# Kernel tuning notes

Measured on AMD Instinct MI355X. Metric: run time of the kernel, lower is better.

Reference implementation:

```python
import jax, jax.numpy as jnp
import numpy as np

HID = 4544; NH = 71; NKV = 1; HD = 64  # Falcon-7B MQA geometry (head_dim hardcoded 64 in _split_heads)
B = 1; U = 32; C = 4; S = 2048          # batch, users, kv chunks, chunk length


def rotate_half(x):
    d = x.shape[-1] // 2
    return jnp.concatenate((-x[..., d:], x[..., :d]), axis=-1)


def setup_inputs() -> dict:
    key = jax.random.key(0)
    ks = jax.random.split(key, 7)
    hidden_states = jax.random.normal(ks[0], (B, U, HID), jnp.float32)
    cos = jax.random.uniform(ks[1], (1, U, 1, HD), jnp.float32, -1.0, 1.0)
    sin = jax.random.uniform(ks[2], (1, U, 1, HD), jnp.float32, -1.0, 1.0)
    k_cache = jax.random.normal(ks[3], (C, B, U, S, HD), jnp.float32)
    v_cache = jax.random.normal(ks[4], (C, B, U, S, HD), jnp.float32)
    attn_masks = jnp.zeros((C, B, U, S), jnp.float32)
    w_qkv = jax.random.normal(ks[5], ((NKV * (NH // NKV + 2)) * HD, HID), jnp.float32) * 0.02
    w_dense = jax.random.normal(ks[6], (HID, HID), jnp.float32) * 0.02
    return {"hidden_states": hidden_states, "cos": cos, "sin": sin,
            "k_cache": k_cache, "v_cache": v_cache, "attn_masks": attn_masks,
            "w_qkv": w_qkv, "w_dense": w_dense}


def reference(hidden_states, cos, sin, k_cache, v_cache, attn_masks, w_qkv, w_dense):
    b, u, _ = hidden_states.shape
    # fused QKV projection (Linear without bias: x @ W.T)
    fused = hidden_states @ w_qkv.T                      # [b,u,(NH+2*NKV)*HD]
    qkv = fused.reshape(b, u, NKV, NH // NKV + 2, HD)    # _split_heads view
    q = qkv[:, :, :, :-2].reshape(b, u, NH, HD)          # query heads
    k_cur = qkv[:, :, :, -2].reshape(b, u, NKV, HD)      # shared MQA key head
    v_cur = qkv[:, :, :, -1].reshape(b, u, NKV, HD)      # shared MQA value head
    # rotary embedding (apply_rotary_pos_emb)
    q = q * cos + rotate_half(q) * sin
    k_cur = k_cur * cos + rotate_half(k_cur) * sin
    inv = 1.0 / jnp.sqrt(jnp.float32(HD))
    # flash-decode over cached chunks: scores [c,b,u,n,s]
    scores = jnp.einsum('bund,cbusd->cbuns', q, k_cache) * inv
    scores = scores + attn_masks[:, :, :, None, :]
    m_c = jnp.max(scores, axis=-1, keepdims=True)        # [c,b,u,n,1] local max
    p = jnp.exp(scores - m_c)
    l_c = jnp.sum(p, axis=-1, keepdims=True)             # local row sums
    # current token = length-1 chunk (its local max is itself, local sum is 1)
    s_cur = jnp.einsum('bund,bued->bune', q, k_cur) * inv  # [b,u,n,1]
    g = jnp.maximum(jnp.max(m_c, axis=0), s_cur)           # global max [b,u,n,1]
    factor = jnp.exp(m_c - g[None])                        # per-chunk rescale
    out = jnp.einsum('cbuns,cbusd->bund', factor * p, v_cache)
    cur_w = jnp.exp(s_cur - g)                             # [b,u,n,1]
    out = out + cur_w * v_cur                              # v_cur broadcasts over heads
    scale = jnp.sum(factor * l_c, axis=0) + cur_w
    out = out / scale
    attn = out.reshape(b, u, NH * HD)
    return attn @ w_dense.T
```

## Files before the change

### kernel.cpp

```cpp
#include <hip/hip_runtime.h>
#include <hip/hip_bf16.h>

typedef __bf16 bf16_t;
typedef __bf16 bf16x8 __attribute__((ext_vector_type(8)));
typedef float  f32x4  __attribute__((ext_vector_type(4)));

#define MFMA16(A,B,C) __builtin_amdgcn_mfma_f32_16x16x32_bf16(A,B,C,0,0,0)

constexpr int HIDc = 4544;
constexpr int NHc  = 71;
constexpr int NHPc = 80;
constexpr int HDc  = 64;
constexpr int Uc   = 32;
constexpr int Sc   = 2048;
constexpr int RQ   = 4672;

constexpr size_t OFF_FUSED = 0;
constexpr size_t OFF_QHI   = 598016;
constexpr size_t OFF_QLO   = 925696;
constexpr size_t OFF_KCUR  = 1253376;
constexpr size_t OFF_VCUR  = 1261568;
constexpr size_t OFF_MP    = 1269760;
constexpr size_t OFF_LP    = 1415168;
constexpr size_t OFF_AHI   = 1560576;
constexpr size_t OFF_ALO   = 1851392;
constexpr size_t OFF_OP    = 2142208;

__device__ __forceinline__ bf16x8 ld8f(const float* base, long eidx) {
  const float* p = base + eidx;
  const f32x4 a = *(const f32x4*)p;
  const f32x4 b = *(const f32x4*)(p + 4);
  bf16x8 r;
  r[0]=(bf16_t)a[0]; r[1]=(bf16_t)a[1]; r[2]=(bf16_t)a[2]; r[3]=(bf16_t)a[3];
  r[4]=(bf16_t)b[0]; r[5]=(bf16_t)b[1]; r[6]=(bf16_t)b[2]; r[7]=(bf16_t)b[3];
  return r;
}

__device__ __forceinline__ void cp16(const float* g, float* l) {
  __builtin_amdgcn_global_load_lds((const __attribute__((address_space(1))) void*)g,
                                   (__attribute__((address_space(3))) void*)l, 16, 0, 0);
}
__device__ __forceinline__ void cp4(const float* g, float* l) {
  __builtin_amdgcn_global_load_lds((const __attribute__((address_space(1))) void*)g,
                                   (__attribute__((address_space(3))) void*)l, 4, 0, 0);
}

__global__ __launch_bounds__(256) void k_zeros(float* fused, float* out) {
  const int i = blockIdx.x*256 + threadIdx.x;
  if (i < Uc*RQ) fused[i] = 0.f;
  else           out[i - Uc*RQ] = 0.f;
}

__global__ __launch_bounds__(256) void k_qkv(
    const float* __restrict__ hidden, const float* __restrict__ wqkv,
    float* __restrict__ fused)
{
  const int h = blockIdx.x, y = blockIdx.y;
  const int t = threadIdx.x;
  const int wave = t >> 6, lane = t & 63;
  const int c = lane & 15, q4 = lane >> 4;
  const int mt = wave & 1, kh = wave >> 1;
  const int ks0 = y*18;
  const int ksn = min(18, 142 - ks0);
  const int h1  = ksn >> 1;
  const int kbeg = ks0 + (kh ? h1 : 0);
  const int kend = ks0 + (kh ? ksn : h1);
  __shared__ float sD[Uc*HDc];

  const long abase = (long)(mt*16 + c)*HIDc + q4*8;
  const long bbase = ((long)h*64 + c)*HIDc + q4*8;
  f32x4 acc[4] = {};
#pragma unroll 3
  for (int ks = kbeg; ks < kend; ++ks) {
    const bf16x8 af = ld8f(hidden, abase + ks*32);
#pragma unroll
    for (int nf = 0; nf < 4; ++nf) {
      const bf16x8 bv = ld8f(wqkv, bbase + (long)nf*16*HIDc + ks*32);
      acc[nf] = MFMA16(af, bv, acc[nf]);
    }
  }
  if (kh == 0) {
#pragma unroll
    for (int r = 0; r < 4; ++r)
#pragma unroll
      for (int nf = 0; nf < 4; ++nf)
        sD[(mt*16 + q4*4 + r)*64 + nf*16 + c] = acc[nf][r];
  }
  __syncthreads();
  if (kh == 1) {
#pragma unroll
    for (int r = 0; r < 4; ++r)
#pragma unroll
      for (int nf = 0; nf < 4; ++nf)
        sD[(mt*16 + q4*4 + r)*64 + nf*16 + c] += acc[nf][r];
  }
  __syncthreads();
  for (int i = t; i < Uc*HDc; i += 256)
    atomicAdd(&fused[(long)(i >> 6)*RQ + h*64 + (i & 63)], sD[i]);
}

__global__ __launch_bounds__(256) void k_rotary(
    const float* __restrict__ fused,
    const float* __restrict__ cosp, const float* __restrict__ sinp,
    bf16_t* __restrict__ qhi, bf16_t* __restrict__ qlo,
    float* __restrict__ kcur, float* __restrict__ vcur)
{
  const int h = blockIdx.x;
  const int t = threadIdx.x;
  __shared__ float sD[Uc*HDc];
  if (h < 73) {
    for (int i = t; i < Uc*HDc; i += 256)
      sD[i] = fused[(long)(i >> 6)*RQ + h*64 + (i & 63)];
    __syncthreads();
  }
  if (h >= NHc) {
    for (int i = t; i < Uc*HDc; i += 256) {
      const long idx = (((long)(i >> 6))*NHPc + h)*HDc + (i & 63);
      qhi[idx] = (bf16_t)0.f;  qlo[idx] = (bf16_t)0.f;
    }
  }
  if (h >= 73) return;
  for (int i = t; i < Uc*HDc; i += 256) {
    const int u = i >> 6, d = i & 63;
    const float x = sD[i];
    const float partner = sD[i ^ 32];
    const float cs = cosp[u*HDc + d];
    const float sn = sinp[u*HDc + d];
    const float rh = (d < 32) ? -partner : partner;
    const float val = x*cs + rh*sn;
    if (h < NHc) {
      const long idx = ((long)u*NHPc + h)*HDc + d;
      const bf16_t hi = (bf16_t)val;
      qhi[idx] = hi;
      qlo[idx] = (bf16_t)(val - (float)hi);
    } else if (h == NHc) {
      kcur[u*HDc + d] = val;
    } else {
      vcur[u*HDc + d] = x;
    }
  }
}

constexpr int ATTN_SLOT_F   = 4096;
constexpr int ATTN_STAGE_F  = 4*ATTN_SLOT_F;
constexpr int ATTN_SMEM_F   = ATTN_STAGE_F + 2048;
constexpr int ATTN_SMEM_BYTES = ATTN_SMEM_F * 4;

__global__ __launch_bounds__(512, 4) void k_attn(
    const float* __restrict__ kc, const float* __restrict__ vc,
    const float* __restrict__ masks,
    const bf16_t* __restrict__ qhi, const bf16_t* __restrict__ qlo,
    float* __restrict__ Mp, float* __restrict__ Lp, float* __restrict__ Op,
    const int NPB)
{
  extern __shared__ float smem[];
  const int u  = blockIdx.x;
  const int pb = blockIdx.y;
  const int tid = threadIdx.x;
  const int wave = __builtin_amdgcn_readfirstlane(tid >> 6);
  const int lane = tid & 63;
  const int c    = lane & 15;
  const int q4   = lane >> 4;
  const int pbpc = NPB >> 2;
  const int keys_pb = 2048 / pbpc;
  const int tcnt    = keys_pb >> 5;
  const int chunk = pb / pbpc;
  const int inner = pb - chunk*pbpc;
  const int s_base = inner*keys_pb;
  const long kvbase = ((long)(chunk*Uc + u))*Sc;

  float* const stage = smem;
  float* const smask = smem + ATTN_STAGE_F;

  const int srow = lane >> 4;
  const int scol = (lane & 15) << 2;

  if (wave >= 5) {
    if (wave == 7) {
      const int nmc = keys_pb >> 6;
      const float* gM = masks + kvbase + s_base;
      for (int i = 0; i < nmc; ++i)
        cp4(gM + i*64 + lane, smask + i*64);
      for (int t = 0; t < tcnt; ++t) {
        __builtin_amdgcn_s_barrier();
        if (t == 0) asm volatile("s_waitcnt vmcnt(0)" ::: "memory");
        __builtin_amdgcn_s_barrier();
      }
      return;
    }
    const float* gsrc = (wave == 5) ? kc : vc;
    const int vofs = (wave == 6) ? 2048 : 0;
    for (int pt = 0; pt < 3; ++pt) {
      const long tb = (kvbase + s_base + pt*32) * 64;
      float* dst = stage + pt*ATTN_SLOT_F + vofs;
#pragma unroll
      for (int i = 0; i < 8; ++i) {
        const int row = i*4 + srow;
        const int fz = ((row & 7) << 2) ^ (((row >> 3) & 1) << 4);
        cp16(gsrc + tb + row*64 + (scol ^ fz), dst + i*256);
      }
    }
    for (int t = 0; t < tcnt; ++t) {
      __builtin_amdgcn_s_barrier();
      if (t + 3 < tcnt) {
        const long tb = (kvbase + s_base + (long)(t+3)*32) * 64;
        float* dst = stage + ((t+3)&3)*ATTN_SLOT_F + vofs;
#pragma unroll
        for (int i = 0; i < 8; ++i) {
          const int row = i*4 + srow;
          const int fz = ((row & 7) << 2) ^ (((row >> 3) & 1) << 4);
          cp16(gsrc + tb + row*64 + (scol ^ fz), dst + i*256);
        }
      }
      const int rem = min(3, tcnt - 1 - t);
      if      (rem >= 3) asm volatile("s_waitcnt vmcnt(24)" ::: "memory");
      else if (rem == 2) asm volatile("s_waitcnt vmcnt(16)" ::: "memory");
      else if (rem == 1) asm volatile("s_waitcnt vmcnt(8)"  ::: "memory");
      else               asm volatile("s_waitcnt vmcnt(0)"  ::: "memory");
      __builtin_amdgcn_s_barrier();
    }
    return;
  }

  const int ht = wave;
  bf16x8 qh[2], ql[2];
  {
    const bf16_t* qb  = qhi + ((long)u*NHPc + ht*16 + c)*HDc + q4*8;
    const bf16_t* qb2 = qlo + ((long)u*NHPc + ht*16 + c)*HDc + q4*8;
#pragma unroll
    for (int ks = 0; ks < 2; ++ks) {
      qh[ks] = *(const bf16x8*)(qb  + ks*32);
      ql[ks] = *(const bf16x8*)(qb2 + ks*32);
    }
  }

  float m_i = -INFINITY, l_i = 0.f;
  f32x4 Oa[4] = {};

  const int krow0 = ((c >> 2) << 3) + (c & 3);

  for (int t = 0; t < tcnt; ++t) {
    __syncthreads();
    __syncthreads();
    float* const lK = stage + (t & 3)*ATTN_SLOT_F;
    float* const lV = lK + 2048;

    bf16x8 kf[2][2];
#pragma unroll
    for (int mt2 = 0; mt2 < 2; ++mt2) {
      const int row = krow0 + mt2*4;
      const int fz = ((row & 7) << 2) ^ (((row >> 3) & 1) << 4);
#pragma unroll
      for (int ks = 0; ks < 2; ++ks) {
        const int b0 = row*64 + ((ks*32 + q4*8) ^ fz);
        const int b1 = row*64 + ((ks*32 + q4*8 + 4) ^ fz);
        const f32x4 a = *(const f32x4*)(lK + b0);
        const f32x4 b = *(const f32x4*)(lK + b1);
        bf16x8 r;
        r[0]=(bf16_t)a[0]; r[1]=(bf16_t)a[1]; r[2]=(bf16_t)a[2]; r[3]=(bf16_t)a[3];
        r[4]=(bf16_t)b[0]; r[5]=(bf16_t)b[1]; r[6]=(bf16_t)b[2]; r[7]=(bf16_t)b[3];
        kf[mt2][ks] = r;
      }
    }

    bf16x8 vf[4];
#pragma unroll
    for (int dt = 0; dt < 4; ++dt) {
      union { bf16_t e[8]; bf16x8 v; } uv;
#pragma unroll
      for (int j = 0; j < 8; ++j) {
        const int row = q4*8 + j;
        const int fz = ((row & 7) << 2) ^ (((row >> 3) & 1) << 4);
        uv.e[j] = (bf16_t)lV[row*64 + ((dt*16 + c) ^ fz)];
      }
      vf[dt] = uv.v;
    }

    f32x4 S[2];
#pragma unroll
    for (int mt2 = 0; mt2 < 2; ++mt2) {
      f32x4 s = {};
      s = MFMA16(kf[mt2][0], qh[0], s);
      s = MFMA16(kf[mt2][1], qh[1], s);
      s = MFMA16(kf[mt2][0], ql[0], s);
      s = MFMA16(kf[mt2][1], ql[1], s);
      S[mt2] = s;
    }

#pragma unroll
    for (int mt2 = 0; mt2 < 2; ++mt2)
#pragma unroll
      for (int r = 0; r < 4; ++r)
        S[mt2][r] = S[mt2][r]*0.125f + smask[t*32 + q4*8 + mt2*4 + r];

    float tm = S[0][0];
#pragma unroll
    for (int mt2 = 0; mt2 < 2; ++mt2)
#pragma unroll
      for (int r = 0; r < 4; ++r) tm = fmaxf(tm, S[mt2][r]);
    tm = fmaxf(tm, __shfl_xor(tm, 16));
    tm = fmaxf(tm, __shfl_xor(tm, 32));
    const float mn = fmaxf(m_i, tm);
    const float alpha = __expf(m_i - mn);
    m_i = mn;
#pragma unroll
    for (int mt2 = 0; mt2 < 2; ++mt2)
#pragma unroll
      for (int r = 0; r < 4; ++r)
        S[mt2][r] = __expf(S[mt2][r] - m_i);
    float rs = 0.f;
#pragma unroll
    for (int mt2 = 0; mt2 < 2; ++mt2)
#pragma unroll
      for (int r = 0; r < 4; ++r) rs += S[mt2][r];
    rs += __shfl_xor(rs, 16);
    rs += __shfl_xor(rs, 32);
    l_i = l_i*alpha + rs;

#pragma unroll
    for (int r = 0; r < 4; ++r) {
      const float ar = __shfl(alpha, q4*4 + r);
#pragma unroll
      for (int dt = 0; dt < 4; ++dt) Oa[dt][r] *= ar;
    }
    bf16x8 ph, pl;
    {
      union { bf16_t e[8]; bf16x8 v; } uh, ul;
#pragma unroll
      for (int j = 0; j < 8; ++j) {
        const float val = (j < 4) ? S[0][j] : S[1][j & 3];
        const bf16_t hi = (bf16_t)val;
        uh.e[j] = hi;
        ul.e[j] = (bf16_t)(val - (float)hi);
      }
      ph = uh.v;  pl = ul.v;
    }
#pragma unroll
    for (int dt = 0; dt < 4; ++dt) {
      Oa[dt] = MFMA16(ph, vf[dt], Oa[dt]);
      Oa[dt] = MFMA16(pl, vf[dt], Oa[dt]);
    }
  }

  float* op = Op + ((long)u*NPB + pb)*NHc*HDc;
#pragma unroll
  for (int dt = 0; dt < 4; ++dt)
#pragma unroll
    for (int r = 0; r < 4; ++r) {
      const int h = ht*16 + q4*4 + r;
      if (h < NHc) op[h*HDc + dt*16 + c] = Oa[dt][r];
    }
  if (q4 == 0) {
    const int hh = ht*16 + c;
    if (hh < NHc) {
      Mp[((long)u*NPB + pb)*NHc + hh] = fmaxf(m_i, -1e30f);
      Lp[((long)u*NPB + pb)*NHc + hh] = l_i;
    }
  }
}

__global__ __launch_bounds__(64) void k_combine(
    const float* __restrict__ Mp, const float* __restrict__ Lp,
    const float* __restrict__ Op,
    const bf16_t* __restrict__ qhi, const bf16_t* __restrict__ qlo,
    const float* __restrict__ kcur, const float* __restrict__ vcur,
    bf16_t* __restrict__ ahi, bf16_t* __restrict__ alo, const int NPB)
{
  const int h = blockIdx.x, u = blockIdx.y;
  const int lane = threadIdx.x;
  const long qidx = ((long)u*NHPc + h)*HDc + lane;
  float pr = ((float)qhi[qidx] + (float)qlo[qidx]) * kcur[u*HDc + lane];
#pragma unroll
  for (int o = 32; o > 0; o >>= 1) pr += __shfl_xor(pr, o);
  const float s_cur = pr * 0.125f;

  float g = s_cur;
  for (int p = 0; p < NPB; ++p)
    g = fmaxf(g, Mp[((long)u*NPB + p)*NHc + h]);
  g = fmaxf(g, -1e30f);
  float sw = 0.f, acc = 0.f;
  const float* ob = Op + (long)u*NPB*NHc*HDc + (long)h*HDc + lane;
  for (int p = 0; p < NPB; ++p) {
    const float f = __expf(Mp[((long)u*NPB + p)*NHc + h] - g);
    sw += f*Lp[((long)u*NPB + p)*NHc + h];
    acc += f*ob[(long)p*NHc*HDc];
  }
  const float cw = __expf(s_cur - g);
  acc += cw * vcur[u*HDc + lane];
  const float attn = acc / (sw + cw);
  const bf16_t hi = (bf16_t)attn;
  ahi[(long)u*HIDc + h*HDc + lane] = hi;
  alo[(long)u*HIDc + h*HDc + lane] = (bf16_t)(attn - (float)hi);
}

__global__ __launch_bounds__(256) void k_outgemm(
    const bf16_t* __restrict__ ahi, const bf16_t* __restrict__ alo,
    const float* __restrict__ wd, float* __restrict__ out)
{
  const int nb = blockIdx.x, y = blockIdx.y;
  const int t = threadIdx.x;
  const int wave = t >> 6, lane = t & 63;
  const int c = lane & 15, q4 = lane >> 4;
  const int mt = wave & 1, kh = wave >> 1;
  const int ks0 = y*18;
  const int ksn = min(18, 142 - ks0);
  const int h1  = ksn >> 1;
  const int kbeg = ks0 + (kh ? h1 : 0);
  const int kend = ks0 + (kh ? ksn : h1);
  __shared__ float sC[Uc*32];

  const bf16_t* aph = ahi + ((long)(mt*16 + c))*HIDc + q4*8;
  const bf16_t* apl = alo + ((long)(mt*16 + c))*HIDc + q4*8;
  const long bbase = ((long)nb*32 + c)*HIDc + q4*8;

  f32x4 acc[2] = {};
#pragma unroll 3
  for (int ks = kbeg; ks < kend; ++ks) {
    const bf16x8 Ah = *(const bf16x8*)(aph + ks*32);
    const bf16x8 Al = *(const bf16x8*)(apl + ks*32);
#pragma unroll
    for (int nf = 0; nf < 2; ++nf) {
      const bf16x8 B = ld8f(wd, bbase + (long)nf*16*HIDc + ks*32);
      acc[nf] = MFMA16(Ah, B, acc[nf]);
      acc[nf] = MFMA16(Al, B, acc[nf]);
    }
  }
  if (kh == 0) {
#pragma unroll
    for (int r = 0; r < 4; ++r)
#pragma unroll
      for (int nf = 0; nf < 2; ++nf)
        sC[(mt*16 + q4*4 + r)*32 + nf*16 + c] = acc[nf][r];
  }
  __syncthreads();
  if (kh == 1) {
#pragma unroll
    for (int r = 0; r < 4; ++r)
#pragma unroll
      for (int nf = 0; nf < 2; ++nf)
        sC[(mt*16 + q4*4 + r)*32 + nf*16 + c] += acc[nf][r];
  }
  __syncthreads();
  for (int i = t; i < Uc*32; i += 256)
    atomicAdd(&out[(long)(i >> 5)*HIDc + nb*32 + (i & 31)], sC[i]);
}

extern "C" void kernel_launch(void* const* d_in, const int* in_sizes, int n_in,
                              void* d_out, int out_size, void* d_ws, size_t ws_size,
                              hipStream_t stream)
{
  const float* hidden = (const float*)d_in[0];
  const float* cosp   = (const float*)d_in[1];
  const float* sinp   = (const float*)d_in[2];
  const float* kcache = (const float*)d_in[3];
  const float* vcache = (const float*)d_in[4];
  const float* masks  = (const float*)d_in[5];
  const float* wqkv   = (const float*)d_in[6];
  const float* wdense = (const float*)d_in[7];
  float* out = (float*)d_out;

  const size_t opb = (size_t)Uc*NHc*HDc*4;
  int NPB = 16;
  if      (ws_size >= OFF_OP + 16*opb) NPB = 16;
  else if (ws_size >= OFF_OP +  8*opb) NPB = 8;
  else if (ws_size >= OFF_OP +  4*opb) NPB = 4;
  else return;

  char* ws = (char*)d_ws;
  float*  fused = (float*)(ws + OFF_FUSED);
  bf16_t* qhi   = (bf16_t*)(ws + OFF_QHI);
  bf16_t* qlo   = (bf16_t*)(ws + OFF_QLO);
  float*  kcur  = (float*)(ws + OFF_KCUR);
  float*  vcur  = (float*)(ws + OFF_VCUR);
  float*  Mp    = (float*)(ws + OFF_MP);
  float*  Lp    = (float*)(ws + OFF_LP);
  bf16_t* ahi   = (bf16_t*)(ws + OFF_AHI);
  bf16_t* alo   = (bf16_t*)(ws + OFF_ALO);
  float*  Op    = (float*)(ws + OFF_OP);

  hipFuncSetAttribute(reinterpret_cast<const void*>(k_attn),
                      hipFuncAttributeMaxDynamicSharedMemorySize, ATTN_SMEM_BYTES);

  k_zeros  <<<1152, 256, 0, stream>>>(fused, out);
  k_qkv    <<<dim3(73, 8), 256, 0, stream>>>(hidden, wqkv, fused);
  k_rotary <<<80, 256, 0, stream>>>(fused, cosp, sinp, qhi, qlo, kcur, vcur);
  k_attn   <<<dim3(32, NPB), 512, ATTN_SMEM_BYTES, stream>>>(kcache, vcache, masks, qhi, qlo, Mp, Lp, Op, NPB);
  k_combine<<<dim3(71, 32), 64, 0, stream>>>(Mp, Lp, Op, qhi, qlo, kcur, vcur, ahi, alo, NPB);
  k_outgemm<<<dim3(142, 8), 256, 0, stream>>>(ahi, alo, wdense, out);
}
```

Before: 334.7 us.

## Process two KV tiles per barrier phase in attention and split rotary over users

```diff
diff --git a/kernel.cpp b/kernel.cpp
--- a/kernel.cpp
+++ b/kernel.cpp
@@ -105,23 +105,24 @@
     bf16_t* __restrict__ qhi, bf16_t* __restrict__ qlo,
     float* __restrict__ kcur, float* __restrict__ vcur)
 {
-  const int h = blockIdx.x;
+  const int h  = blockIdx.x;
+  const int u0 = blockIdx.y*8;
   const int t = threadIdx.x;
-  __shared__ float sD[Uc*HDc];
+  __shared__ float sD[8*HDc];
   if (h < 73) {
-    for (int i = t; i < Uc*HDc; i += 256)
-      sD[i] = fused[(long)(i >> 6)*RQ + h*64 + (i & 63)];
+    for (int i = t; i < 8*HDc; i += 256)
+      sD[i] = fused[(long)(u0 + (i >> 6))*RQ + h*64 + (i & 63)];
     __syncthreads();
   }
   if (h >= NHc) {
-    for (int i = t; i < Uc*HDc; i += 256) {
-      const long idx = (((long)(i >> 6))*NHPc + h)*HDc + (i & 63);
+    for (int i = t; i < 8*HDc; i += 256) {
+      const long idx = (((long)(u0 + (i >> 6)))*NHPc + h)*HDc + (i & 63);
       qhi[idx] = (bf16_t)0.f;  qlo[idx] = (bf16_t)0.f;
     }
   }
   if (h >= 73) return;
-  for (int i = t; i < Uc*HDc; i += 256) {
-    const int u = i >> 6, d = i & 63;
+  for (int i = t; i < 8*HDc; i += 256) {
+    const int u = u0 + (i >> 6), d = i & 63;
     const float x = sD[i];
     const float partner = sD[i ^ 32];
     const float cs = cosp[u*HDc + d];
@@ -163,7 +164,7 @@
   const int q4   = lane >> 4;
   const int pbpc = NPB >> 2;
   const int keys_pb = 2048 / pbpc;
-  const int tcnt    = keys_pb >> 5;
+  const int ph_cnt  = keys_pb >> 6;
   const int chunk = pb / pbpc;
   const int inner = pb - chunk*pbpc;
   const int s_base = inner*keys_pb;
@@ -181,18 +182,19 @@
       const float* gM = masks + kvbase + s_base;
       for (int i = 0; i < nmc; ++i)
         cp4(gM + i*64 + lane, smask + i*64);
-      for (int t = 0; t < tcnt; ++t) {
+      for (int p = 0; p < ph_cnt; ++p) {
         __builtin_amdgcn_s_barrier();
-        if (t == 0) asm volatile("s_waitcnt vmcnt(0)" ::: "memory");
+        if (p == 0) asm volatile("s_waitcnt vmcnt(0)" ::: "memory");
         __builtin_amdgcn_s_barrier();
       }
       return;
     }
     const float* gsrc = (wave == 5) ? kc : vc;
     const int vofs = (wave == 6) ? 2048 : 0;
-    for (int pt = 0; pt < 3; ++pt) {
-      const long tb = (kvbase + s_base + pt*32) * 64;
-      float* dst = stage + pt*ATTN_SLOT_F + vofs;
+#pragma unroll
+    for (int sl = 0; sl < 2; ++sl) {
+      const long tb = (kvbase + s_base + sl*32) * 64;
+      float* dst = stage + sl*ATTN_SLOT_F + vofs;
 #pragma unroll
       for (int i = 0; i < 8; ++i) {
         const int row = i*4 + srow;
@@ -200,23 +202,25 @@
         cp16(gsrc + tb + row*64 + (scol ^ fz), dst + i*256);
       }
     }
-    for (int t = 0; t < tcnt; ++t) {
+    for (int p = 0; p < ph_cnt; ++p) {
       __builtin_amdgcn_s_barrier();
-      if (t + 3 < tcnt) {
-        const long tb = (kvbase + s_base + (long)(t+3)*32) * 64;
-        float* dst = stage + ((t+3)&3)*ATTN_SLOT_F + vofs;
-#pragma unroll
-        for (int i = 0; i < 8; ++i) {
-          const int row = i*4 + srow;
-          const int fz = ((row & 7) << 2) ^ (((row >> 3) & 1) << 4);
-          cp16(gsrc + tb + row*64 + (scol ^ fz), dst + i*256);
+      if (p + 1 < ph_cnt) {
+        const int g = ((p+1) & 1)*2;
+#pragma unroll
+        for (int sl = 0; sl < 2; ++sl) {
+          const long tb = (kvbase + s_base + (long)(p+1)*64 + sl*32) * 64;
+          float* dst = stage + (g + sl)*ATTN_SLOT_F + vofs;
+#pragma unroll
+          for (int i = 0; i < 8; ++i) {
+            const int row = i*4 + srow;
+            const int fz = ((row & 7) << 2) ^ (((row >> 3) & 1) << 4);
+            cp16(gsrc + tb + row*64 + (scol ^ fz), dst + i*256);
+          }
         }
-      }
-      const int rem = min(3, tcnt - 1 - t);
-      if      (rem >= 3) asm volatile("s_waitcnt vmcnt(24)" ::: "memory");
-      else if (rem == 2) asm volatile("s_waitcnt vmcnt(16)" ::: "memory");
-      else if (rem == 1) asm volatile("s_waitcnt vmcnt(8)"  ::: "memory");
-      else               asm volatile("s_waitcnt vmcnt(0)"  ::: "memory");
+        asm volatile("s_waitcnt vmcnt(16)" ::: "memory");
+      } else {
+        asm volatile("s_waitcnt vmcnt(0)" ::: "memory");
+      }
       __builtin_amdgcn_s_barrier();
     }
     return;
@@ -239,80 +243,77 @@
 
   const int krow0 = ((c >> 2) << 3) + (c & 3);
 
-  for (int t = 0; t < tcnt; ++t) {
+  for (int p = 0; p < ph_cnt; ++p) {
     __syncthreads();
     __syncthreads();
-    float* const lK = stage + (t & 3)*ATTN_SLOT_F;
-    float* const lV = lK + 2048;
-
-    bf16x8 kf[2][2];
-#pragma unroll
-    for (int mt2 = 0; mt2 < 2; ++mt2) {
-      const int row = krow0 + mt2*4;
-      const int fz = ((row & 7) << 2) ^ (((row >> 3) & 1) << 4);
-#pragma unroll
-      for (int ks = 0; ks < 2; ++ks) {
-        const int b0 = row*64 + ((ks*32 + q4*8) ^ fz);
-        const int b1 = row*64 + ((ks*32 + q4*8 + 4) ^ fz);
-        const f32x4 a = *(const f32x4*)(lK + b0);
-        const f32x4 b = *(const f32x4*)(lK + b1);
-        bf16x8 r;
-        r[0]=(bf16_t)a[0]; r[1]=(bf16_t)a[1]; r[2]=(bf16_t)a[2]; r[3]=(bf16_t)a[3];
-        r[4]=(bf16_t)b[0]; r[5]=(bf16_t)b[1]; r[6]=(bf16_t)b[2]; r[7]=(bf16_t)b[3];
-        kf[mt2][ks] = r;
-      }
-    }
-
-    bf16x8 vf[4];
-#pragma unroll
-    for (int dt = 0; dt < 4; ++dt) {
-      union { bf16_t e[8]; bf16x8 v; } uv;
-#pragma unroll
-      for (int j = 0; j < 8; ++j) {
-        const int row = q4*8 + j;
+    const int g = (p & 1)*2;
+
+    f32x4 S[2][2];
+    __builtin_amdgcn_s_setprio(1);
+#pragma unroll
+    for (int h2 = 0; h2 < 2; ++h2) {
+      float* const lK = stage + (g + h2)*ATTN_SLOT_F;
+#pragma unroll
+      for (int mt2 = 0; mt2 < 2; ++mt2) {
+        const int row = krow0 + mt2*4;
         const int fz = ((row & 7) << 2) ^ (((row >> 3) & 1) << 4);
-        uv.e[j] = (bf16_t)lV[row*64 + ((dt*16 + c) ^ fz)];
-      }
-      vf[dt] = uv.v;
-    }
-
-    f32x4 S[2];
-#pragma unroll
-    for (int mt2 = 0; mt2 < 2; ++mt2) {
-      f32x4 s = {};
-      s = MFMA16(kf[mt2][0], qh[0], s);
-      s = MFMA16(kf[mt2][1], qh[1], s);
-      s = MFMA16(kf[mt2][0], ql[0], s);
-      s = MFMA16(kf[mt2][1], ql[1], s);
-      S[mt2] = s;
-    }
-
-#pragma unroll
-    for (int mt2 = 0; mt2 < 2; ++mt2)
-#pragma unroll
-      for (int r = 0; r < 4; ++r)
-        S[mt2][r] = S[mt2][r]*0.125f + smask[t*32 + q4*8 + mt2*4 + r];
-
-    float tm = S[0][0];
-#pragma unroll
-    for (int mt2 = 0; mt2 < 2; ++mt2)
-#pragma unroll
-      for (int r = 0; r < 4; ++r) tm = fmaxf(tm, S[mt2][r]);
+        bf16x8 k0, k1;
+#pragma unroll
+        for (int ks = 0; ks < 2; ++ks) {
+          const int b0 = row*64 + ((ks*32 + q4*8) ^ fz);
+          const int b1 = row*64 + ((ks*32 + q4*8 + 4) ^ fz);
+          const f32x4 a = *(const f32x4*)(lK + b0);
+          const f32x4 b = *(const f32x4*)(lK + b1);
+          bf16x8 r;
+          r[0]=(bf16_t)a[0]; r[1]=(bf16_t)a[1]; r[2]=(bf16_t)a[2]; r[3]=(bf16_t)a[3];
+          r[4]=(bf16_t)b[0]; r[5]=(bf16_t)b[1]; r[6]=(bf16_t)b[2]; r[7]=(bf16_t)b[3];
+          if (ks == 0) k0 = r; else k1 = r;
+        }
+        f32x4 s = {};
+        s = MFMA16(k0, qh[0], s);
+        s = MFMA16(k1, qh[1], s);
+        s = MFMA16(k0, ql[0], s);
+        s = MFMA16(k1, ql[1], s);
+        S[h2][mt2] = s;
+      }
+    }
+    __builtin_amdgcn_s_setprio(0);
+
+#pragma unroll
+    for (int h2 = 0; h2 < 2; ++h2)
+#pragma unroll
+      for (int mt2 = 0; mt2 < 2; ++mt2)
+#pragma unroll
+        for (int r = 0; r < 4; ++r)
+          S[h2][mt2][r] = S[h2][mt2][r]*0.125f
+                        + smask[p*64 + h2*32 + q4*8 + mt2*4 + r];
+
+    float tm = S[0][0][0];
+#pragma unroll
+    for (int h2 = 0; h2 < 2; ++h2)
+#pragma unroll
+      for (int mt2 = 0; mt2 < 2; ++mt2)
+#pragma unroll
+        for (int r = 0; r < 4; ++r) tm = fmaxf(tm, S[h2][mt2][r]);
     tm = fmaxf(tm, __shfl_xor(tm, 16));
     tm = fmaxf(tm, __shfl_xor(tm, 32));
     const float mn = fmaxf(m_i, tm);
     const float alpha = __expf(m_i - mn);
     m_i = mn;
 #pragma unroll
-    for (int mt2 = 0; mt2 < 2; ++mt2)
-#pragma unroll
-      for (int r = 0; r < 4; ++r)
-        S[mt2][r] = __expf(S[mt2][r] - m_i);
+    for (int h2 = 0; h2 < 2; ++h2)
+#pragma unroll
+      for (int mt2 = 0; mt2 < 2; ++mt2)
+#pragma unroll
+        for (int r = 0; r < 4; ++r)
+          S[h2][mt2][r] = __expf(S[h2][mt2][r] - m_i);
     float rs = 0.f;
 #pragma unroll
-    for (int mt2 = 0; mt2 < 2; ++mt2)
-#pragma unroll
-      for (int r = 0; r < 4; ++r) rs += S[mt2][r];
+    for (int h2 = 0; h2 < 2; ++h2)
+#pragma unroll
+      for (int mt2 = 0; mt2 < 2; ++mt2)
+#pragma unroll
+        for (int r = 0; r < 4; ++r) rs += S[h2][mt2][r];
     rs += __shfl_xor(rs, 16);
     rs += __shfl_xor(rs, 32);
     l_i = l_i*alpha + rs;
@@ -323,22 +324,41 @@
 #pragma unroll
       for (int dt = 0; dt < 4; ++dt) Oa[dt][r] *= ar;
     }
-    bf16x8 ph, pl;
-    {
-      union { bf16_t e[8]; bf16x8 v; } uh, ul;
-#pragma unroll
-      for (int j = 0; j < 8; ++j) {
-        const float val = (j < 4) ? S[0][j] : S[1][j & 3];
-        const bf16_t hi = (bf16_t)val;
-        uh.e[j] = hi;
-        ul.e[j] = (bf16_t)(val - (float)hi);
-      }
-      ph = uh.v;  pl = ul.v;
-    }
-#pragma unroll
-    for (int dt = 0; dt < 4; ++dt) {
-      Oa[dt] = MFMA16(ph, vf[dt], Oa[dt]);
-      Oa[dt] = MFMA16(pl, vf[dt], Oa[dt]);
+
+#pragma unroll
+    for (int h2 = 0; h2 < 2; ++h2) {
+      float* const lV = stage + (g + h2)*ATTN_SLOT_F + 2048;
+      bf16x8 vf[4];
+#pragma unroll
+      for (int dt = 0; dt < 4; ++dt) {
+        union { bf16_t e[8]; bf16x8 v; } uv;
+#pragma unroll
+        for (int j = 0; j < 8; ++j) {
+          const int row = q4*8 + j;
+          const int fz = ((row & 7) << 2) ^ (((row >> 3) & 1) << 4);
+          uv.e[j] = (bf16_t)lV[row*64 + ((dt*16 + c) ^ fz)];
+        }
+        vf[dt] = uv.v;
+      }
+      bf16x8 ph, pl;
+      {
+        union { bf16_t e[8]; bf16x8 v; } uh, ul;
+#pragma unroll
+        for (int j = 0; j < 8; ++j) {
+          const float val = (j < 4) ? S[h2][0][j] : S[h2][1][j & 3];
+          const bf16_t hi = (bf16_t)val;
+          uh.e[j] = hi;
+          ul.e[j] = (bf16_t)(val - (float)hi);
+        }
+        ph = uh.v;  pl = ul.v;
+      }
+      __builtin_amdgcn_s_setprio(1);
+#pragma unroll
+      for (int dt = 0; dt < 4; ++dt) {
+        Oa[dt] = MFMA16(ph, vf[dt], Oa[dt]);
+        Oa[dt] = MFMA16(pl, vf[dt], Oa[dt]);
+      }
+      __builtin_amdgcn_s_setprio(0);
     }
   }
 
@@ -483,7 +503,7 @@
 
   k_zeros  <<<1152, 256, 0, stream>>>(fused, out);
   k_qkv    <<<dim3(73, 8), 256, 0, stream>>>(hidden, wqkv, fused);
-  k_rotary <<<80, 256, 0, stream>>>(fused, cosp, sinp, qhi, qlo, kcur, vcur);
+  k_rotary <<<dim3(80, 4), 256, 0, stream>>>(fused, cosp, sinp, qhi, qlo, kcur, vcur);
   k_attn   <<<dim3(32, NPB), 512, ATTN_SMEM_BYTES, stream>>>(kcache, vcache, masks, qhi, qlo, Mp, Lp, Op, NPB);
   k_combine<<<dim3(71, 32), 64, 0, stream>>>(Mp, Lp, Op, qhi, qlo, kcur, vcur, ahi, alo, NPB);
   k_outgemm<<<dim3(142, 8), 256, 0, stream>>>(ahi, alo, wdense, out);
```

Result: no change. 337.8 us (+0.9%).
